# Kernel optimization log

Measured on AMD Instinct MI355X. Metric: run time of the kernel, lower is better.

The kernel has to match this reference:

```python
import jax, jax.numpy as jnp
import numpy as np
from jax import lax

COST_CLASS, COST_BBOX, COST_GIOU = 1.0, 5.0, 2.0
BIG = 1e30  # stand-in for +inf when masking assigned rows/cols


def box_cxcywh_to_xyxy(b):
    cx, cy, w, h = b[..., 0], b[..., 1], b[..., 2], b[..., 3]
    return jnp.stack([cx - 0.5 * w, cy - 0.5 * h, cx + 0.5 * w, cy + 0.5 * h], axis=-1)


def generalized_box_iou(boxes1, boxes2):
    # boxes1: [Q,4] xyxy, boxes2: [T,4] xyxy -> [Q,T]
    area1 = jnp.clip(boxes1[:, 2] - boxes1[:, 0], 0) * jnp.clip(boxes1[:, 3] - boxes1[:, 1], 0)
    area2 = jnp.clip(boxes2[:, 2] - boxes2[:, 0], 0) * jnp.clip(boxes2[:, 3] - boxes2[:, 1], 0)
    lt = jnp.maximum(boxes1[:, None, :2], boxes2[None, :, :2])
    rb = jnp.minimum(boxes1[:, None, 2:], boxes2[None, :, 2:])
    wh = jnp.clip(rb - lt, 0)
    inter = wh[..., 0] * wh[..., 1]
    union = area1[:, None] + area2[None, :] - inter
    iou = inter / jnp.clip(union, 1e-6)
    lt_e = jnp.minimum(boxes1[:, None, :2], boxes2[None, :, :2])
    rb_e = jnp.maximum(boxes1[:, None, 2:], boxes2[None, :, 2:])
    wh_e = jnp.clip(rb_e - lt_e, 0)
    area = wh_e[..., 0] * wh_e[..., 1]
    return iou - (area - union) / jnp.clip(area, 1e-6)


def build_cost(pred_logits, pred_boxes, tgt_labels, tgt_boxes):
    # pred_logits [B,Q,C], pred_boxes [B,Q,4] cxcywh, tgt_labels [B,T], tgt_boxes [B,T,4]
    B, Q, C = pred_logits.shape
    T = tgt_labels.shape[1]
    out_prob = jax.nn.softmax(pred_logits, axis=-1)                       # [B,Q,C]
    idx = jnp.broadcast_to(tgt_labels[:, None, :], (B, Q, T))
    cost_class = -jnp.take_along_axis(out_prob, idx, axis=2)              # [B,Q,T]
    cost_bbox = jnp.sum(jnp.abs(pred_boxes[:, :, None, :] - tgt_boxes[:, None, :, :]), axis=-1)
    giou = jax.vmap(generalized_box_iou)(box_cxcywh_to_xyxy(pred_boxes), box_cxcywh_to_xyxy(tgt_boxes))
    return COST_CLASS * cost_class + COST_BBOX * cost_bbox + COST_GIOU * (-giou)


def greedy_assignment(cost):
    # cost [Q,T] -> (src_idx [n], tgt_idx [n]) with n = min(Q,T); GPU-resident scan
    Q, T = cost.shape
    n = min(Q, T)

    def step(c, _):
        flat = jnp.argmin(c)
        i = flat // T
        j = flat % T
        c = c.at[i, :].set(BIG).at[:, j].set(BIG)
        return c, (i.astype(jnp.int64), j.astype(jnp.int64))

    _, (src, tgt) = lax.scan(step, cost, None, length=n)
    return src, tgt


def setup_inputs() -> dict:
    key = jax.random.key(0)
    k1, k2, k3, k4 = jax.random.split(key, 4)
    B, Q, C, T = 64, 900, 256, 100
    pred_logits = jax.random.normal(k1, (B, Q, C), dtype=jnp.float32)
    pred_boxes = jax.random.uniform(k2, (B, Q, 4), dtype=jnp.float32)   # cxcywh in [0,1)
    tgt_labels = jax.random.randint(k3, (B, T), 0, C)
    tgt_boxes = jax.random.uniform(k4, (B, T, 4), dtype=jnp.float32)
    return {"pred_logits": pred_logits, "pred_boxes": pred_boxes,
            "tgt_labels": tgt_labels, "tgt_boxes": tgt_boxes}


def reference(pred_logits, pred_boxes, tgt_labels, tgt_boxes):
    cost = build_cost(pred_logits, pred_boxes, tgt_labels, tgt_boxes)   # [B,Q,T]
    src_idx, tgt_idx = jax.vmap(greedy_assignment)(cost)                # [B,n] each
    return cost, src_idx, tgt_idx
```

## Files before the change

kernel.cpp:

```cpp
#include <hip/hip_runtime.h>
#include <math.h>

#define B_ 64
#define Q_ 900
#define C_ 256
#define T_ 100
#define N_ 100
#define BIGF 1.0e30f
#define ROWS_PER_LANE 15
#define CHUNKS 25
#define RPC 36

typedef unsigned int u32;
typedef unsigned long long ull;

__device__ inline u32 hm_ordf(float v) {
    u32 u = __float_as_uint(v);
    return (u & 0x80000000u) ? ~u : (u | 0x80000000u);
}
__device__ inline ull hm_ikey(float v, int r, int t) {
    return ~(((ull)hm_ordf(v) << 18) | ((ull)(u32)r << 7) | (ull)(u32)t);
}

__global__ __launch_bounds__(256) void hm_cost_colmin_f32(
    const float* __restrict__ logits,
    const float* __restrict__ pboxes,
    const int*   __restrict__ tlabels,
    const float* __restrict__ tboxes,
    float* __restrict__ cost,
    ull* __restrict__ part)
{
    int bc   = blockIdx.x;
    int b    = bc / CHUNKS;
    int c    = bc % CHUNKS;
    int lane = threadIdx.x & 63;
    int wid  = threadIdx.x >> 6;
    int r0   = c * RPC;

    __shared__ float s_exp[4][C_];
    __shared__ ull   s_part[4][128][2];

    int ta = lane, tb = 64 + lane;
    bool hb = (tb < T_);
    int laba = tlabels[b * T_ + ta];
    int labb = hb ? tlabels[b * T_ + tb] : 0;
    const float* tba = tboxes + ((size_t)b * T_ + ta) * 4;
    const float* tbb = tboxes + ((size_t)b * T_ + (hb ? tb : 0)) * 4;
    float tcxa = tba[0], tcya = tba[1], twa = tba[2], tha = tba[3];
    float tcxb = tbb[0], tcyb = tbb[1], twb = tbb[2], thb_ = tbb[3];
    float txa1 = tcxa - 0.5f * twa, tya1 = tcya - 0.5f * tha;
    float txa2 = tcxa + 0.5f * twa, tya2 = tcya + 0.5f * tha;
    float txb1 = tcxb - 0.5f * twb, tyb1 = tcyb - 0.5f * thb_;
    float txb2 = tcxb + 0.5f * twb, tyb2 = tcyb + 0.5f * thb_;
    float area2a = fmaxf(txa2 - txa1, 0.0f) * fmaxf(tya2 - tya1, 0.0f);
    float area2b = fmaxf(txb2 - txb1, 0.0f) * fmaxf(tyb2 - tyb1, 0.0f);

    ull ka1 = 0ull, ka2 = 0ull;
    ull kb1 = 0ull, kb2 = 0ull;

    for (int r = r0 + wid; r < r0 + RPC; r += 4) {
        int bq = b * Q_ + r;

        const float* row = logits + (size_t)bq * C_;
        float v[4];
        float m = -INFINITY;
#pragma unroll
        for (int i = 0; i < 4; ++i) {
            v[i] = row[lane + 64 * i];
            m = fmaxf(m, v[i]);
        }
#pragma unroll
        for (int off = 32; off >= 1; off >>= 1)
            m = fmaxf(m, __shfl_xor(m, off, 64));

        float e[4];
        float s = 0.0f;
#pragma unroll
        for (int i = 0; i < 4; ++i) {
            e[i] = expf(v[i] - m);
            s += e[i];
        }
#pragma unroll
        for (int off = 32; off >= 1; off >>= 1)
            s += __shfl_xor(s, off, 64);

#pragma unroll
        for (int i = 0; i < 4; ++i)
            s_exp[wid][lane + 64 * i] = e[i];

        const float* pb = pboxes + (size_t)bq * 4;
        float pcx = pb[0], pcy = pb[1], pw = pb[2], ph = pb[3];
        float px1 = pcx - 0.5f * pw, py1 = pcy - 0.5f * ph;
        float px2 = pcx + 0.5f * pw, py2 = pcy + 0.5f * ph;
        float area1 = fmaxf(px2 - px1, 0.0f) * fmaxf(py2 - py1, 0.0f);

        {
            float prob = s_exp[wid][laba] / s;
            float l1 = fabsf(pcx - tcxa) + fabsf(pcy - tcya) + fabsf(pw - twa) + fabsf(ph - tha);
            float iw = fmaxf(fminf(px2, txa2) - fmaxf(px1, txa1), 0.0f);
            float ih = fmaxf(fminf(py2, tya2) - fmaxf(py1, tya1), 0.0f);
            float inter = iw * ih;
            float uni = area1 + area2a - inter;
            float iou = inter / fmaxf(uni, 1e-6f);
            float ew = fmaxf(fmaxf(px2, txa2) - fminf(px1, txa1), 0.0f);
            float eh = fmaxf(fmaxf(py2, tya2) - fminf(py1, tya1), 0.0f);
            float earea = ew * eh;
            float giou = iou - (earea - uni) / fmaxf(earea, 1e-6f);
            float cf = -prob + 5.0f * l1 - 2.0f * giou;
            cost[(size_t)bq * T_ + ta] = cf;
            ull kk = hm_ikey(cf, r, ta);
            if (kk > ka1) { ka2 = ka1; ka1 = kk; }
            else if (kk > ka2) ka2 = kk;
        }
        if (hb) {
            float prob = s_exp[wid][labb] / s;
            float l1 = fabsf(pcx - tcxb) + fabsf(pcy - tcyb) + fabsf(pw - twb) + fabsf(ph - thb_);
            float iw = fmaxf(fminf(px2, txb2) - fmaxf(px1, txb1), 0.0f);
            float ih = fmaxf(fminf(py2, tyb2) - fmaxf(py1, tyb1), 0.0f);
            float inter = iw * ih;
            float uni = area1 + area2b - inter;
            float iou = inter / fmaxf(uni, 1e-6f);
            float ew = fmaxf(fmaxf(px2, txb2) - fminf(px1, txb1), 0.0f);
            float eh = fmaxf(fmaxf(py2, tyb2) - fminf(py1, tyb1), 0.0f);
            float earea = ew * eh;
            float giou = iou - (earea - uni) / fmaxf(earea, 1e-6f);
            float cf = -prob + 5.0f * l1 - 2.0f * giou;
            cost[(size_t)bq * T_ + tb] = cf;
            ull kk = hm_ikey(cf, r, tb);
            if (kk > kb1) { kb2 = kb1; kb1 = kk; }
            else if (kk > kb2) kb2 = kk;
        }
    }

    s_part[wid][lane][0]      = ka1;
    s_part[wid][lane][1]      = ka2;
    s_part[wid][64 + lane][0] = kb1;
    s_part[wid][64 + lane][1] = kb2;
    __syncthreads();
    int tid = threadIdx.x;
    if (tid < T_) {
        ull b1 = 0ull, b2 = 0ull;
#pragma unroll
        for (int w = 0; w < 4; ++w) {
#pragma unroll
            for (int j = 0; j < 2; ++j) {
                ull cc = s_part[w][tid][j];
                if (cc > b1) { b2 = b1; b1 = cc; }
                else if (cc > b2) b2 = cc;
            }
        }
        ull* dst = part + (((size_t)b * CHUNKS + c) * T_ + tid) * 2;
        dst[0] = b1;
        dst[1] = b2;
    }
}

__device__ inline u32 hm_umax32(u32 a, u32 b) { return a > b ? a : b; }

__device__ inline u32 hm_wave_max_u32_full(u32 y) {
    y = hm_umax32(y, (u32)__builtin_amdgcn_update_dpp(0, (int)y, 0x111, 0xF, 0xF, false));
    y = hm_umax32(y, (u32)__builtin_amdgcn_update_dpp(0, (int)y, 0x112, 0xF, 0xF, false));
    y = hm_umax32(y, (u32)__builtin_amdgcn_update_dpp(0, (int)y, 0x114, 0xF, 0xF, false));
    y = hm_umax32(y, (u32)__builtin_amdgcn_update_dpp(0, (int)y, 0x118, 0xF, 0xF, false));
    y = hm_umax32(y, (u32)__builtin_amdgcn_update_dpp(0, (int)y, 0x142, 0xF, 0xF, false));
    y = hm_umax32(y, (u32)__builtin_amdgcn_update_dpp(0, (int)y, 0x143, 0xF, 0xF, false));
    return (u32)__builtin_amdgcn_readlane((int)y, 63);
}

template <int CTRL>
__device__ inline ull hm_dpp64(ull x) {
    u32 lo = (u32)x, hi = (u32)(x >> 32);
    lo = (u32)__builtin_amdgcn_update_dpp(0, (int)lo, CTRL, 0xF, 0xF, false);
    hi = (u32)__builtin_amdgcn_update_dpp(0, (int)hi, CTRL, 0xF, 0xF, false);
    return ((ull)hi << 32) | lo;
}
__device__ inline ull hm_wave_max_full64(ull x) {
    ull p;
    p = hm_dpp64<0x111>(x); x = (p > x) ? p : x;
    p = hm_dpp64<0x112>(x); x = (p > x) ? p : x;
    p = hm_dpp64<0x114>(x); x = (p > x) ? p : x;
    p = hm_dpp64<0x118>(x); x = (p > x) ? p : x;
    p = hm_dpp64<0x142>(x); x = (p > x) ? p : x;
    p = hm_dpp64<0x143>(x); x = (p > x) ? p : x;
    u32 lo = (u32)__builtin_amdgcn_readlane((int)(u32)x, 63);
    u32 hi = (u32)__builtin_amdgcn_readlane((int)(u32)(x >> 32), 63);
    return ((ull)hi << 32) | lo;
}

__global__ __launch_bounds__(64) void hm_greedy_32(
    const float* __restrict__ cost,
    const ull* __restrict__ part,
    float* __restrict__ out_src,
    float* __restrict__ out_tgt)
{
    int b = blockIdx.x;
    int l = threadIdx.x;
    const float* Cb = cost + (size_t)b * Q_ * T_;

    int  t0 = l, t1 = 64 + l;
    bool a1 = (t1 < T_);

    ull c1a = 0ull, c2a = 0ull, c1b = 0ull, c2b = 0ull;
#pragma unroll
    for (int c = 0; c < CHUNKS; ++c) {
        const ull* p0 = part + (((size_t)b * CHUNKS + c) * T_ + t0) * 2;
#pragma unroll
        for (int j = 0; j < 2; ++j) {
            ull cc = p0[j];
            if (cc > c1a) { c2a = c1a; c1a = cc; }
            else if (cc > c2a) c2a = cc;
        }
        if (a1) {
            const ull* p1 = part + (((size_t)b * CHUNKS + c) * T_ + t1) * 2;
#pragma unroll
            for (int j = 0; j < 2; ++j) {
                ull cc = p1[j];
                if (cc > c1b) { c2b = c1b; c1b = cc; }
                else if (cc > c2b) c2b = cc;
            }
        }
    }
    u32 va  = (u32)((~c1a) >> 18), ida  = (u32)(~c1a) & 0x3FFFFu;
    u32 v2a = (u32)((~c2a) >> 18), id2a = (u32)(~c2a) & 0x3FFFFu;
    u32 vb  = a1 ? (u32)((~c1b) >> 18) : 0xFFFFFFFFu;
    u32 idb = a1 ? ((u32)(~c1b) & 0x3FFFFu) : 0x3FFFFu;
    u32 v2b = a1 ? (u32)((~c2b) >> 18) : 0xFFFFFFFFu;
    u32 id2b = a1 ? ((u32)(~c2b) & 0x3FFFFu) : 0x3FFFFu;

    unsigned removed = 0u;
    u32 pk0 = 0u, pk1 = 0u;

    int k = 0;
    while (k < N_) {
        u32 ya = ~va, yb = ~vb;
        u32 winy = hm_wave_max_u32_full(ya > yb ? ya : yb);

        u32 za = (ya == winy) ? ~ida : 0u;
        u32 zb = (yb == winy) ? ~idb : 0u;
        u32 winz = hm_wave_max_u32_full(za > zb ? za : zb);
        u32 winid = (~winz) & 0x3FFFFu;

        int t = (int)(winid & 127u);
        int q = (int)((winid >> 7) & 1023u);

        if (winid & 0x20000u) {
            ull b1 = 0ull, b2 = 0ull;
#pragma unroll
            for (int i = 0; i < ROWS_PER_LANE; ++i) {
                int r = l + 64 * i;
                bool ok = (r < Q_) && !((removed >> i) & 1u);
                float v = ok ? Cb[(size_t)r * T_ + t] : BIGF;
                ull ik = ok ? hm_ikey(v, r, t) : 0ull;
                if (ik > b1) { b2 = b1; b1 = ik; }
                else if (ik > b2) b2 = ik;
            }
            ull w1 = hm_wave_max_full64(b1);
            ull alt = (b1 == w1) ? b2 : b1;
            ull w2 = hm_wave_max_full64(alt);
            if (t0 == t) {
                va  = (u32)((~w1) >> 18); ida  = (u32)(~w1) & 0x3FFFFu;
                v2a = (u32)((~w2) >> 18); id2a = (u32)(~w2) & 0x3FFFFu;
            }
            if (t1 == t) {
                vb  = (u32)((~w1) >> 18); idb  = (u32)(~w1) & 0x3FFFFu;
                v2b = (u32)((~w2) >> 18); id2b = (u32)(~w2) & 0x3FFFFu;
            }
            continue;
        }

        u32 qt = winid & 0x1FFFFu;
        if (k < 64) { if (l == k)        pk0 = qt; }
        else        { if (l == (k & 63)) pk1 = qt; }
        if ((q & 63) == l) removed |= 1u << (q >> 6);

        {
            bool die1 = (((ida  >> 7) & 1023u) == (u32)q);
            bool die2 = (((id2a >> 7) & 1023u) == (u32)q);
            u32 nva  = die1 ? v2a  : va;
            u32 nida = die1 ? id2a : ida;
            u32 nid2 = (die1 || die2) ? (id2a | 0x20000u) : id2a;
            bool kill = (t0 == t);
            va   = kill ? 0xFFFFFFFFu : nva;
            ida  = kill ? 0x3FFFFu    : nida;
            v2a  = kill ? 0xFFFFFFFFu : v2a;
            id2a = kill ? 0x3FFFFu    : nid2;
        }
        {
            bool die1 = (((idb  >> 7) & 1023u) == (u32)q);
            bool die2 = (((id2b >> 7) & 1023u) == (u32)q);
            u32 nvb  = die1 ? v2b  : vb;
            u32 nidb = die1 ? id2b : idb;
            u32 nid2 = (die1 || die2) ? (id2b | 0x20000u) : id2b;
            bool kill = (t1 == t);
            vb   = kill ? 0xFFFFFFFFu : nvb;
            idb  = kill ? 0x3FFFFu    : nidb;
            v2b  = kill ? 0xFFFFFFFFu : v2b;
            id2b = kill ? 0x3FFFFu    : nid2;
        }

        ++k;
    }

    float* os = out_src + b * N_;
    float* ot = out_tgt + b * N_;
    os[l] = (float)(pk0 >> 7);
    ot[l] = (float)(pk0 & 127u);
    if (l < N_ - 64) {
        os[64 + l] = (float)(pk1 >> 7);
        ot[64 + l] = (float)(pk1 & 127u);
    }
}

extern "C" void kernel_launch(void* const* d_in, const int* in_sizes, int n_in,
                              void* d_out, int out_size, void* d_ws, size_t ws_size,
                              hipStream_t stream)
{
    const float* pred_logits = (const float*)d_in[0];
    const float* pred_boxes  = (const float*)d_in[1];
    const int*   tgt_labels  = (const int*)d_in[2];
    const float* tgt_boxes   = (const float*)d_in[3];

    float* out_cost = (float*)d_out;
    float* out_src  = out_cost + (size_t)B_ * Q_ * T_;
    float* out_tgt  = out_src  + (size_t)B_ * N_;

    ull* part = (ull*)d_ws;

    hm_cost_colmin_f32<<<B_ * CHUNKS, 256, 0, stream>>>(pred_logits, pred_boxes,
                                                        tgt_labels, tgt_boxes,
                                                        out_cost, part);

    hm_greedy_32<<<B_, 64, 0, stream>>>(out_cost, part, out_src, out_tgt);
}
```

Before: 89.19 us.

## Fuse cost and greedy kernels with per-batch atomic counter handoff

Merges the cost/column-min kernel and the greedy assignment kernel into one launch. The extra blocks at the end of the grid spin on a per-batch atomic counter until all chunks for their batch finish, so the greedy work for early batches can overlap cost computation for later ones. A small zeroing kernel is added to reset counters. This trades the inter-kernel gap for spin-waiting blocks and relies on the greedy blocks being scheduled after their producers to avoid deadlock.

```diff
diff --git a/kernel.cpp b/kernel.cpp
--- a/kernel.cpp
+++ b/kernel.cpp
@@ -20,139 +20,6 @@
 }
 __device__ inline ull hm_ikey(float v, int r, int t) {
     return ~(((ull)hm_ordf(v) << 18) | ((ull)(u32)r << 7) | (ull)(u32)t);
-}
-
-__global__ __launch_bounds__(256) void hm_cost_colmin_f32(
-    const float* __restrict__ logits,
-    const float* __restrict__ pboxes,
-    const int*   __restrict__ tlabels,
-    const float* __restrict__ tboxes,
-    float* __restrict__ cost,
-    ull* __restrict__ part)
-{
-    int bc   = blockIdx.x;
-    int b    = bc / CHUNKS;
-    int c    = bc % CHUNKS;
-    int lane = threadIdx.x & 63;
-    int wid  = threadIdx.x >> 6;
-    int r0   = c * RPC;
-
-    __shared__ float s_exp[4][C_];
-    __shared__ ull   s_part[4][128][2];
-
-    int ta = lane, tb = 64 + lane;
-    bool hb = (tb < T_);
-    int laba = tlabels[b * T_ + ta];
-    int labb = hb ? tlabels[b * T_ + tb] : 0;
-    const float* tba = tboxes + ((size_t)b * T_ + ta) * 4;
-    const float* tbb = tboxes + ((size_t)b * T_ + (hb ? tb : 0)) * 4;
-    float tcxa = tba[0], tcya = tba[1], twa = tba[2], tha = tba[3];
-    float tcxb = tbb[0], tcyb = tbb[1], twb = tbb[2], thb_ = tbb[3];
-    float txa1 = tcxa - 0.5f * twa, tya1 = tcya - 0.5f * tha;
-    float txa2 = tcxa + 0.5f * twa, tya2 = tcya + 0.5f * tha;
-    float txb1 = tcxb - 0.5f * twb, tyb1 = tcyb - 0.5f * thb_;
-    float txb2 = tcxb + 0.5f * twb, tyb2 = tcyb + 0.5f * thb_;
-    float area2a = fmaxf(txa2 - txa1, 0.0f) * fmaxf(tya2 - tya1, 0.0f);
-    float area2b = fmaxf(txb2 - txb1, 0.0f) * fmaxf(tyb2 - tyb1, 0.0f);
-
-    ull ka1 = 0ull, ka2 = 0ull;
-    ull kb1 = 0ull, kb2 = 0ull;
-
-    for (int r = r0 + wid; r < r0 + RPC; r += 4) {
-        int bq = b * Q_ + r;
-
-        const float* row = logits + (size_t)bq * C_;
-        float v[4];
-        float m = -INFINITY;
-#pragma unroll
-        for (int i = 0; i < 4; ++i) {
-            v[i] = row[lane + 64 * i];
-            m = fmaxf(m, v[i]);
-        }
-#pragma unroll
-        for (int off = 32; off >= 1; off >>= 1)
-            m = fmaxf(m, __shfl_xor(m, off, 64));
-
-        float e[4];
-        float s = 0.0f;
-#pragma unroll
-        for (int i = 0; i < 4; ++i) {
-            e[i] = expf(v[i] - m);
-            s += e[i];
-        }
-#pragma unroll
-        for (int off = 32; off >= 1; off >>= 1)
-            s += __shfl_xor(s, off, 64);
-
-#pragma unroll
-        for (int i = 0; i < 4; ++i)
-            s_exp[wid][lane + 64 * i] = e[i];
-
-        const float* pb = pboxes + (size_t)bq * 4;
-        float pcx = pb[0], pcy = pb[1], pw = pb[2], ph = pb[3];
-        float px1 = pcx - 0.5f * pw, py1 = pcy - 0.5f * ph;
-        float px2 = pcx + 0.5f * pw, py2 = pcy + 0.5f * ph;
-        float area1 = fmaxf(px2 - px1, 0.0f) * fmaxf(py2 - py1, 0.0f);
-
-        {
-            float prob = s_exp[wid][laba] / s;
-            float l1 = fabsf(pcx - tcxa) + fabsf(pcy - tcya) + fabsf(pw - twa) + fabsf(ph - tha);
-            float iw = fmaxf(fminf(px2, txa2) - fmaxf(px1, txa1), 0.0f);
-            float ih = fmaxf(fminf(py2, tya2) - fmaxf(py1, tya1), 0.0f);
-            float inter = iw * ih;
-            float uni = area1 + area2a - inter;
-            float iou = inter / fmaxf(uni, 1e-6f);
-            float ew = fmaxf(fmaxf(px2, txa2) - fminf(px1, txa1), 0.0f);
-            float eh = fmaxf(fmaxf(py2, tya2) - fminf(py1, tya1), 0.0f);
-            float earea = ew * eh;
-            float giou = iou - (earea - uni) / fmaxf(earea, 1e-6f);
-            float cf = -prob + 5.0f * l1 - 2.0f * giou;
-            cost[(size_t)bq * T_ + ta] = cf;
-            ull kk = hm_ikey(cf, r, ta);
-            if (kk > ka1) { ka2 = ka1; ka1 = kk; }
-            else if (kk > ka2) ka2 = kk;
-        }
-        if (hb) {
-            float prob = s_exp[wid][labb] / s;
-            float l1 = fabsf(pcx - tcxb) + fabsf(pcy - tcyb) + fabsf(pw - twb) + fabsf(ph - thb_);
-            float iw = fmaxf(fminf(px2, txb2) - fmaxf(px1, txb1), 0.0f);
-            float ih = fmaxf(fminf(py2, tyb2) - fmaxf(py1, tyb1), 0.0f);
-            float inter = iw * ih;
-            float uni = area1 + area2b - inter;
-            float iou = inter / fmaxf(uni, 1e-6f);
-            float ew = fmaxf(fmaxf(px2, txb2) - fminf(px1, txb1), 0.0f);
-            float eh = fmaxf(fmaxf(py2, tyb2) - fminf(py1, tyb1), 0.0f);
-            float earea = ew * eh;
-            float giou = iou - (earea - uni) / fmaxf(earea, 1e-6f);
-            float cf = -prob + 5.0f * l1 - 2.0f * giou;
-            cost[(size_t)bq * T_ + tb] = cf;
-            ull kk = hm_ikey(cf, r, tb);
-            if (kk > kb1) { kb2 = kb1; kb1 = kk; }
-            else if (kk > kb2) kb2 = kk;
-        }
-    }
-
-    s_part[wid][lane][0]      = ka1;
-    s_part[wid][lane][1]      = ka2;
-    s_part[wid][64 + lane][0] = kb1;
-    s_part[wid][64 + lane][1] = kb2;
-    __syncthreads();
-    int tid = threadIdx.x;
-    if (tid < T_) {
-        ull b1 = 0ull, b2 = 0ull;
-#pragma unroll
-        for (int w = 0; w < 4; ++w) {
-#pragma unroll
-            for (int j = 0; j < 2; ++j) {
-                ull cc = s_part[w][tid][j];
-                if (cc > b1) { b2 = b1; b1 = cc; }
-                else if (cc > b2) b2 = cc;
-            }
-        }
-        ull* dst = part + (((size_t)b * CHUNKS + c) * T_ + tid) * 2;
-        dst[0] = b1;
-        dst[1] = b2;
-    }
 }
 
 __device__ inline u32 hm_umax32(u32 a, u32 b) { return a > b ? a : b; }
@@ -187,15 +54,166 @@
     return ((ull)hi << 32) | lo;
 }
 
-__global__ __launch_bounds__(64) void hm_greedy_32(
-    const float* __restrict__ cost,
-    const ull* __restrict__ part,
+__global__ void hm_zero(int* __restrict__ cnt) {
+    if (threadIdx.x < B_) cnt[threadIdx.x] = 0;
+}
+
+__global__ __launch_bounds__(256) void hm_fused(
+    const float* __restrict__ logits,
+    const float* __restrict__ pboxes,
+    const int*   __restrict__ tlabels,
+    const float* __restrict__ tboxes,
+    float* __restrict__ cost,
+    ull* __restrict__ part,
+    int* __restrict__ cnt,
     float* __restrict__ out_src,
     float* __restrict__ out_tgt)
 {
-    int b = blockIdx.x;
+    int bc = blockIdx.x;
+
+    if (bc < B_ * CHUNKS) {
+        int b    = bc / CHUNKS;
+        int c    = bc % CHUNKS;
+        int lane = threadIdx.x & 63;
+        int wid  = threadIdx.x >> 6;
+        int r0   = c * RPC;
+
+        __shared__ float s_exp[4][C_];
+        __shared__ ull   s_part[4][128][2];
+
+        int ta = lane, tb = 64 + lane;
+        bool hb = (tb < T_);
+        int laba = tlabels[b * T_ + ta];
+        int labb = hb ? tlabels[b * T_ + tb] : 0;
+        const float* tba = tboxes + ((size_t)b * T_ + ta) * 4;
+        const float* tbb = tboxes + ((size_t)b * T_ + (hb ? tb : 0)) * 4;
+        float tcxa = tba[0], tcya = tba[1], twa = tba[2], tha = tba[3];
+        float tcxb = tbb[0], tcyb = tbb[1], twb = tbb[2], thb_ = tbb[3];
+        float txa1 = tcxa - 0.5f * twa, tya1 = tcya - 0.5f * tha;
+        float txa2 = tcxa + 0.5f * twa, tya2 = tcya + 0.5f * tha;
+        float txb1 = tcxb - 0.5f * twb, tyb1 = tcyb - 0.5f * thb_;
+        float txb2 = tcxb + 0.5f * twb, tyb2 = tcyb + 0.5f * thb_;
+        float area2a = fmaxf(txa2 - txa1, 0.0f) * fmaxf(tya2 - tya1, 0.0f);
+        float area2b = fmaxf(txb2 - txb1, 0.0f) * fmaxf(tyb2 - tyb1, 0.0f);
+
+        ull ka1 = 0ull, ka2 = 0ull;
+        ull kb1 = 0ull, kb2 = 0ull;
+
+        for (int r = r0 + wid; r < r0 + RPC; r += 4) {
+            int bq = b * Q_ + r;
+
+            const float* row = logits + (size_t)bq * C_;
+            float v[4];
+            float m = -INFINITY;
+#pragma unroll
+            for (int i = 0; i < 4; ++i) {
+                v[i] = row[lane + 64 * i];
+                m = fmaxf(m, v[i]);
+            }
+#pragma unroll
+            for (int off = 32; off >= 1; off >>= 1)
+                m = fmaxf(m, __shfl_xor(m, off, 64));
+
+            float e[4];
+            float s = 0.0f;
+#pragma unroll
+            for (int i = 0; i < 4; ++i) {
+                e[i] = expf(v[i] - m);
+                s += e[i];
+            }
+#pragma unroll
+            for (int off = 32; off >= 1; off >>= 1)
+                s += __shfl_xor(s, off, 64);
+
+#pragma unroll
+            for (int i = 0; i < 4; ++i)
+                s_exp[wid][lane + 64 * i] = e[i];
+
+            const float* pb = pboxes + (size_t)bq * 4;
+            float pcx = pb[0], pcy = pb[1], pw = pb[2], ph = pb[3];
+            float px1 = pcx - 0.5f * pw, py1 = pcy - 0.5f * ph;
+            float px2 = pcx + 0.5f * pw, py2 = pcy + 0.5f * ph;
+            float area1 = fmaxf(px2 - px1, 0.0f) * fmaxf(py2 - py1, 0.0f);
+
+            {
+                float prob = s_exp[wid][laba] / s;
+                float l1 = fabsf(pcx - tcxa) + fabsf(pcy - tcya) + fabsf(pw - twa) + fabsf(ph - tha);
+                float iw = fmaxf(fminf(px2, txa2) - fmaxf(px1, txa1), 0.0f);
+                float ih = fmaxf(fminf(py2, tya2) - fmaxf(py1, tya1), 0.0f);
+                float inter = iw * ih;
+                float uni = area1 + area2a - inter;
+                float iou = inter / fmaxf(uni, 1e-6f);
+                float ew = fmaxf(fmaxf(px2, txa2) - fminf(px1, txa1), 0.0f);
+                float eh = fmaxf(fmaxf(py2, tya2) - fminf(py1, tya1), 0.0f);
+                float earea = ew * eh;
+                float giou = iou - (earea - uni) / fmaxf(earea, 1e-6f);
+                float cf = -prob + 5.0f * l1 - 2.0f * giou;
+                cost[(size_t)bq * T_ + ta] = cf;
+                ull kk = hm_ikey(cf, r, ta);
+                if (kk > ka1) { ka2 = ka1; ka1 = kk; }
+                else if (kk > ka2) ka2 = kk;
+            }
+            if (hb) {
+                float prob = s_exp[wid][labb] / s;
+                float l1 = fabsf(pcx - tcxb) + fabsf(pcy - tcyb) + fabsf(pw - twb) + fabsf(ph - thb_);
+                float iw = fmaxf(fminf(px2, txb2) - fmaxf(px1, txb1), 0.0f);
+                float ih = fmaxf(fminf(py2, tyb2) - fmaxf(py1, tyb1), 0.0f);
+                float inter = iw * ih;
+                float uni = area1 + area2b - inter;
+                float iou = inter / fmaxf(uni, 1e-6f);
+                float ew = fmaxf(fmaxf(px2, txb2) - fminf(px1, txb1), 0.0f);
+                float eh = fmaxf(fmaxf(py2, tyb2) - fminf(py1, tyb1), 0.0f);
+                float earea = ew * eh;
+                float giou = iou - (earea - uni) / fmaxf(earea, 1e-6f);
+                float cf = -prob + 5.0f * l1 - 2.0f * giou;
+                cost[(size_t)bq * T_ + tb] = cf;
+                ull kk = hm_ikey(cf, r, tb);
+                if (kk > kb1) { kb2 = kb1; kb1 = kk; }
+                else if (kk > kb2) kb2 = kk;
+            }
+        }
+
+        s_part[wid][lane][0]      = ka1;
+        s_part[wid][lane][1]      = ka2;
+        s_part[wid][64 + lane][0] = kb1;
+        s_part[wid][64 + lane][1] = kb2;
+        __syncthreads();
+        int tid = threadIdx.x;
+        if (tid < T_) {
+            ull b1 = 0ull, b2 = 0ull;
+#pragma unroll
+            for (int w = 0; w < 4; ++w) {
+#pragma unroll
+                for (int j = 0; j < 2; ++j) {
+                    ull cc = s_part[w][tid][j];
+                    if (cc > b1) { b2 = b1; b1 = cc; }
+                    else if (cc > b2) b2 = cc;
+                }
+            }
+            ull* dst = part + (((size_t)b * CHUNKS + c) * T_ + tid) * 2;
+            dst[0] = b1;
+            dst[1] = b2;
+        }
+
+        __syncthreads();
+        if (threadIdx.x == 0) {
+            __threadfence();
+            __hip_atomic_fetch_add(&cnt[b], 1, __ATOMIC_RELEASE,
+                                   __HIP_MEMORY_SCOPE_AGENT);
+        }
+        return;
+    }
+
+    if (threadIdx.x >= 64) return;
+    int b = bc - B_ * CHUNKS;
     int l = threadIdx.x;
     const float* Cb = cost + (size_t)b * Q_ * T_;
+
+    while (__hip_atomic_load(&cnt[b], __ATOMIC_ACQUIRE,
+                             __HIP_MEMORY_SCOPE_AGENT) < CHUNKS) {
+        __builtin_amdgcn_s_sleep(2);
+    }
+    __threadfence();
 
     int  t0 = l, t1 = 64 + l;
     bool a1 = (t1 < T_);
@@ -325,10 +343,11 @@
     float* out_tgt  = out_src  + (size_t)B_ * N_;
 
     ull* part = (ull*)d_ws;
-
-    hm_cost_colmin_f32<<<B_ * CHUNKS, 256, 0, stream>>>(pred_logits, pred_boxes,
-                                                        tgt_labels, tgt_boxes,
-                                                        out_cost, part);
-
-    hm_greedy_32<<<B_, 64, 0, stream>>>(out_cost, part, out_src, out_tgt);
-}
+    int* cnt  = (int*)(part + (size_t)B_ * CHUNKS * T_ * 2);
+
+    hm_zero<<<1, 64, 0, stream>>>(cnt);
+
+    hm_fused<<<B_ * CHUNKS + B_, 256, 0, stream>>>(
+        pred_logits, pred_boxes, tgt_labels, tgt_boxes,
+        out_cost, part, cnt, out_src, out_tgt);
+}
```

New measurement: 176.0 us. 1.97x slower.
